# Performance work log

Measured on AMD Instinct MI355X. Metric: run time of the kernel, lower is better.

## Reference

```python
import jax, jax.numpy as jnp
import numpy as np

N, D, F, E, TOP_K = 8192, 1024, 2048, 8, 2


def setup_inputs() -> dict:
    key = jax.random.key(0)
    ks = jax.random.split(key, 8)
    s = 0.02
    x = jax.random.normal(ks[0], (N, D), dtype=jnp.float32)
    Wr = jax.random.normal(ks[1], (D, E), dtype=jnp.float32) * s  # router
    br = jnp.zeros((E,), jnp.float32)
    W1 = jax.random.normal(ks[2], (E, D, F), dtype=jnp.float32) * s  # expert FFN in
    b1 = jnp.zeros((E, F), jnp.float32)
    W2 = jax.random.normal(ks[3], (E, F, D), dtype=jnp.float32) * s  # expert FFN out
    b2 = jnp.zeros((E, D), jnp. float32)
    return {"x": x, "Wr": Wr, "br": br, "W1": W1, "b1": b1, "W2": W2, "b2": b2}


def reference(x, Wr, br, W1, b1, W2, b2):
    # Router: per-token expert logits -> softmax probabilities -> top-k sampler.
    logits = x @ Wr + br                         # [N, E]
    probs = jax.nn.softmax(logits, axis=-1)      # [N, E]
    top_p, top_i = jax.lax.top_k(probs, TOP_K)   # [N, K]
    # Combine weights: prob mass only on the selected top-k experts per token.
    w = (jax.nn.one_hot(top_i, E, dtype=x.dtype) * top_p[..., None]).sum(axis=1)  # [N, E]
    # Per-expert gather-compute-scatter, expressed as masked full-batch expert FFN
    # (identical math: tokens not routed to expert e have weight 0).
    out = jnp.zeros((x.shape[0], W2.shape[-1]), dtype=x.dtype)
    for e in range(E):  # small fixed loop over structurally distinct experts
        h = jax.nn.gelu(x @ W1[e] + b1[e])       # [N, F]
        y = h @ W2[e] + b2[e]                    # [N, D]
        out = out + w[:, e:e + 1] * y            # weighted scatter-add combine
    return out
```

## Files before the change

### kernel.cpp

```cpp
#include <hip/hip_runtime.h>
#include <hip/hip_bf16.h>


#define N_TOK 8192
#define DIM   1024
#define FF    2048
#define NE    8

typedef unsigned short ushort_t;
typedef __bf16 bf16x8 __attribute__((ext_vector_type(8)));
typedef float  f32x4  __attribute__((ext_vector_type(4)));
typedef unsigned short u16x8 __attribute__((ext_vector_type(8)));

__device__ __forceinline__ ushort_t f2bf(float f) {
    union { float f; unsigned int u; } v; v.f = f;
    unsigned int r = (v.u + 0x7FFFu + ((v.u >> 16) & 1u)) >> 16;
    return (ushort_t)r;
}

__device__ __forceinline__ void gload_lds16(const ushort_t* g, ushort_t* l) {
    __builtin_amdgcn_global_load_lds(
        (const __attribute__((address_space(1))) void*)g,
        (__attribute__((address_space(3))) void*)l,
        16, 0, 0);
}

__global__ __launch_bounds__(256) void convert_x_kernel(
    const float* __restrict__ x, ushort_t* __restrict__ xb)
{
    size_t i = ((size_t)blockIdx.x * 256 + threadIdx.x) * 8;
    float4 a = *reinterpret_cast<const float4*>(x + i);
    float4 b = *reinterpret_cast<const float4*>(x + i + 4);
    u16x8 o;
    o[0] = f2bf(a.x); o[1] = f2bf(a.y); o[2] = f2bf(a.z); o[3] = f2bf(a.w);
    o[4] = f2bf(b.x); o[5] = f2bf(b.y); o[6] = f2bf(b.z); o[7] = f2bf(b.w);
    *reinterpret_cast<u16x8*>(xb + i) = o;
}

__global__ __launch_bounds__(256) void transpose_conv_kernel(
    const float* __restrict__ in, ushort_t* __restrict__ out, int R, int C)
{
    __shared__ float tile[64][68];
    const int e = blockIdx.z;
    const float* I = in + (size_t)e * R * C;
    ushort_t*    O = out + (size_t)e * R * C;
    const int c0 = blockIdx.x * 64, r0 = blockIdx.y * 64;
    const int tid = threadIdx.x;
#pragma unroll
    for (int j = 0; j < 4; ++j) {
        int row = j * 16 + (tid >> 4);
        int col = (tid & 15) * 4;
        float4 v = *reinterpret_cast<const float4*>(&I[(size_t)(r0 + row) * C + c0 + col]);
        *reinterpret_cast<float4*>(&tile[row][col]) = v;
    }
    __syncthreads();
#pragma unroll
    for (int j = 0; j < 2; ++j) {
        int orow = j * 32 + (tid >> 3);
        int k0   = (tid & 7) * 8;
        u16x8 o;
#pragma unroll
        for (int k = 0; k < 8; ++k) o[k] = f2bf(tile[k0 + k][orow]);
        *reinterpret_cast<u16x8*>(&O[(size_t)(c0 + orow) * R + r0 + k0]) = o;
    }
}

__global__ __launch_bounds__(256) void router_kernel(
    const float* __restrict__ x, const float* __restrict__ Wr, const float* __restrict__ br,
    int* __restrict__ cnt, int* __restrict__ tok_list, float* __restrict__ w_list)
{
    __shared__ int   se0[64], se1[64];
    __shared__ float sw0[64], sw1[64];

    const int wid  = threadIdx.x >> 6;
    const int lane = threadIdx.x & 63;
    const int tblk = blockIdx.x * 64;

    for (int i = 0; i < 16; ++i) {
        const int li = wid * 16 + i;
        const int t  = tblk + li;
        const float* xr = x + (size_t)t * DIM;

        float acc[NE];
#pragma unroll
        for (int e = 0; e < NE; ++e) acc[e] = 0.f;
        for (int d = lane; d < DIM; d += 64) {
            float xv = xr[d];
            const float4* w4 = reinterpret_cast<const float4*>(Wr + (size_t)d * NE);
            float4 w0 = w4[0], w1 = w4[1];
            acc[0] += xv * w0.x; acc[1] += xv * w0.y; acc[2] += xv * w0.z; acc[3] += xv * w0.w;
            acc[4] += xv * w1.x; acc[5] += xv * w1.y; acc[6] += xv * w1.z; acc[7] += xv * w1.w;
        }
#pragma unroll
        for (int e = 0; e < NE; ++e) {
            for (int off = 32; off > 0; off >>= 1)
                acc[e] += __shfl_down(acc[e], off, 64);
        }
        if (lane == 0) {
            float l[NE];
#pragma unroll
            for (int e = 0; e < NE; ++e) l[e] = acc[e] + br[e];
            float mx = l[0];
#pragma unroll
            for (int e = 1; e < NE; ++e) mx = fmaxf(mx, l[e]);
            float p[NE], s = 0.f;
#pragma unroll
            for (int e = 0; e < NE; ++e) { p[e] = expf(l[e] - mx); s += p[e]; }
            float inv = 1.f / s;
            int e0 = 0;
#pragma unroll
            for (int e = 1; e < NE; ++e) if (l[e] > l[e0]) e0 = e;
            int e1 = (e0 == 0) ? 1 : 0;
#pragma unroll
            for (int e = 0; e < NE; ++e) if (e != e0 && l[e] > l[e1]) e1 = e;
            se0[li] = e0; sw0[li] = p[e0] * inv;
            se1[li] = e1; sw1[li] = p[e1] * inv;
        }
    }
    __syncthreads();

    if (threadIdx.x < 64) {
        const int t  = tblk + lane;
        const int e0 = se0[lane], e1 = se1[lane];
        const unsigned long long below = ((unsigned long long)1 << lane) - 1;
        int p0 = 0, p1 = 0;
#pragma unroll
        for (int e = 0; e < NE; ++e) {
            unsigned long long m0 = __ballot(e0 == e);
            unsigned long long m1 = __ballot(e1 == e);
            int c = __popcll(m0) + __popcll(m1);
            int b = 0;
            if (lane == e && c) b = atomicAdd(&cnt[e], c);
            b = __shfl(b, e, 64);
            if (e0 == e) p0 = b + __popcll(m0 & below);
            if (e1 == e) p1 = b + __popcll(m0) + __popcll(m1 & below);
        }
        tok_list[e0 * N_TOK + p0] = t;  w_list[e0 * N_TOK + p0] = sw0[lane];
        tok_list[e1 * N_TOK + p1] = t;  w_list[e1 * N_TOK + p1] = sw1[lane];
    }
}

__global__ void scan_kernel(const int* __restrict__ cnt, int* __restrict__ offs,
                            int* __restrict__ tile_e, int* __restrict__ tile_m0,
                            int* __restrict__ meta)
{
    if (threadIdx.x == 0 && blockIdx.x == 0) {
        int s = 0;
        for (int e = 0; e < NE; ++e) { offs[e] = s; s += cnt[e]; }
        offs[NE] = s;
        int nt = 0;
        for (int e = 0; e < NE; ++e)
            for (int m0 = 0; m0 < cnt[e]; m0 += 128) {
                tile_e[nt] = e; tile_m0[nt] = m0; ++nt;
            }
        meta[0] = nt;
    }
}

template <int MODE>
__global__ __launch_bounds__(512, 6) void moe_gemm_kernel(
    const ushort_t* __restrict__ A,
    const ushort_t* __restrict__ Bt,
    const float*    __restrict__ bias,
    const int*      __restrict__ cnt,
    const int*      __restrict__ offs,
    const int*      __restrict__ tok_list,
    const float*    __restrict__ w_list,
    const int*      __restrict__ tile_e,
    const int*      __restrict__ tile_m0,
    const int*      __restrict__ meta,
    ushort_t*       __restrict__ hout,
    float*          __restrict__ out)
{
    const int K    = (MODE == 0) ? 1024 : 2048;
    const int NCOL = (MODE == 0) ? 2048 : 1024;

    const int nmt = meta[0];
    const int L   = nmt << 4;

    const int xcd = blockIdx.x & 7;
    const int q = L >> 3, r = L & 7;
    const int cstart = (xcd < r) ? xcd * (q + 1) : r * (q + 1) + (xcd - r) * q;
    const int clen   = (xcd < r) ? q + 1 : q;

    __shared__ ushort_t As[3][128 * 32];
    __shared__ ushort_t Bs[3][128 * 32];

    const int tid  = threadIdx.x;
    const int lane = tid & 63;
    const int wid  = tid >> 6;
    const int wr = (wid >> 2) * 64;
    const int wc = (wid & 3) * 32;
    const int la = lane & 15;
    const int kc = lane >> 4;

    for (int i = blockIdx.x >> 3; i < clen; i += 96) {
        const int tau = cstart + i;
        const int mt  = tau >> 4;
        int nb, kh;
        if (MODE == 0) { nb = tau & 15; kh = 0; }
        else           { kh = tau & 1;  nb = (tau >> 1) & 7; }
        const int e   = tile_e[mt];
        const int m0  = tile_m0[mt];
        const int cnt_e  = cnt[e];
        const int offs_e = offs[e];
        const int n0  = nb * 128;
        const int koff = kh << 10;

        __syncthreads();

        const int srow  = tid >> 2;
        const int chunk = (tid & 3) ^ ((srow >> 1) & 3);
        size_t asrc, bsrc;
        {
            int entry = m0 + srow;
            if (MODE == 0) {
                int tok = (entry < cnt_e) ? tok_list[e * N_TOK + entry] : 0;
                asrc = (size_t)tok * K + chunk * 8;
            } else {
                asrc = (size_t)(offs_e + entry) * K + koff + chunk * 8;
            }
            bsrc = ((size_t)e * NCOL + n0 + srow) * K + koff + chunk * 8;
        }

        f32x4 acc[4][2];
#pragma unroll
        for (int m = 0; m < 4; ++m)
#pragma unroll
            for (int n = 0; n < 2; ++n)
                acc[m][n] = (f32x4){0.f, 0.f, 0.f, 0.f};

        auto STAGE = [&](int t, int b) {
            int k0 = t * 32;
            gload_lds16(A  + asrc + k0, &As[b][tid * 8]);
            gload_lds16(Bt + bsrc + k0, &Bs[b][tid * 8]);
        };

        auto COMPUTE = [&](int b) {
            bf16x8 af[4], bfr[2];
#pragma unroll
            for (int m = 0; m < 4; ++m) {
                int rr = wr + m * 16 + la;
                af[m] = *reinterpret_cast<const bf16x8*>(&As[b][(rr * 4 + (kc ^ ((rr >> 1) & 3))) * 8]);
            }
#pragma unroll
            for (int n = 0; n < 2; ++n) {
                int rr = wc + n * 16 + la;
                bfr[n] = *reinterpret_cast<const bf16x8*>(&Bs[b][(rr * 4 + (kc ^ ((rr >> 1) & 3))) * 8]);
            }
            __builtin_amdgcn_s_setprio(1);
#pragma unroll
            for (int m = 0; m < 4; ++m)
#pragma unroll
                for (int n = 0; n < 2; ++n)
                    acc[m][n] = __builtin_amdgcn_mfma_f32_16x16x32_bf16(af[m], bfr[n], acc[m][n], 0, 0, 0);
            __builtin_amdgcn_s_setprio(0);
        };

        const int nk = 32;
        STAGE(0, 0);
        STAGE(1, 1);
        for (int t = 0; t < nk - 1; ++t) {
            asm volatile("s_waitcnt vmcnt(2)" ::: "memory");
            __builtin_amdgcn_s_barrier();
            if (t + 2 < nk) STAGE(t + 2, (t + 2) % 3);
            COMPUTE(t % 3);
        }
        asm volatile("s_waitcnt vmcnt(0)" ::: "memory");
        __builtin_amdgcn_s_barrier();
        COMPUTE((nk - 1) % 3);

#pragma unroll
        for (int m = 0; m < 4; ++m) {
            int rbase = wr + m * 16 + (lane >> 4) * 4;
#pragma unroll
            for (int n = 0; n < 2; ++n) {
                int gcol = n0 + wc + n * 16 + la;
                float bi = (MODE == 1 && kh != 0) ? 0.f : bias[(size_t)e * NCOL + gcol];
#pragma unroll
                for (int jj = 0; jj < 4; ++jj) {
                    int entry = m0 + rbase + jj;
                    if (entry < cnt_e) {
                        float v = acc[m][n][jj] + bi;
                        if (MODE == 0) {
                            float u = 0.7978845608028654f * (v + 0.044715f * v * v * v);
                            float t2 = __builtin_amdgcn_exp2f(2.8853900817779268f * u);
                            float g = v * (t2 / (t2 + 1.f));
                            hout[(size_t)(offs_e + entry) * FF + gcol] = f2bf(g);
                        } else {
                            int tok  = tok_list[e * N_TOK + entry];
                            float w  = w_list  [e * N_TOK + entry];
                            atomicAdd(&out[(size_t)tok * DIM + gcol], w * v);
                        }
                    }
                }
            }
        }
    }
}

extern "C" void kernel_launch(void* const* d_in, const int* in_sizes, int n_in,
                              void* d_out, int out_size, void* d_ws, size_t ws_size,
                              hipStream_t stream)
{
    const float* x  = (const float*)d_in[0];
    const float* Wr = (const float*)d_in[1];
    const float* br = (const float*)d_in[2];
    const float* W1 = (const float*)d_in[3];
    const float* b1 = (const float*)d_in[4];
    const float* W2 = (const float*)d_in[5];
    const float* b2 = (const float*)d_in[6];
    float* out = (float*)d_out;

    char* ws = (char*)d_ws;
    size_t off = 0;
    auto alloc = [&](size_t bytes) -> void* {
        void* p = ws + off;
        off = (off + bytes + 255) & ~(size_t)255;
        return p;
    };
    ushort_t* w1t = (ushort_t*)alloc((size_t)NE * DIM * FF * 2);
    ushort_t* w2t = (ushort_t*)alloc((size_t)NE * DIM * FF * 2);
    ushort_t* xb  = (ushort_t*)alloc((size_t)N_TOK * DIM * 2);
    ushort_t* h   = (ushort_t*)alloc(((size_t)2 * N_TOK + 128) * FF * 2);
    int*      cnt = (int*)alloc(NE * sizeof(int));
    int*      offs= (int*)alloc((NE + 1) * sizeof(int));
    int*   tok_list = (int*)alloc((size_t)NE * N_TOK * sizeof(int));
    float* w_list   = (float*)alloc((size_t)NE * N_TOK * sizeof(float));
    int*   tile_e   = (int*)alloc(256 * sizeof(int));
    int*   tile_m0  = (int*)alloc(256 * sizeof(int));
    int*   meta     = (int*)alloc(16 * sizeof(int));
    (void)ws_size; (void)in_sizes; (void)n_in;

    hipMemsetAsync(out, 0, (size_t)out_size * sizeof(float), stream);
    hipMemsetAsync(cnt, 0, NE * sizeof(int), stream);

    convert_x_kernel<<<(N_TOK * DIM) / (8 * 256), 256, 0, stream>>>(x, xb);
    transpose_conv_kernel<<<dim3(FF / 64, DIM / 64, NE), 256, 0, stream>>>(W1, w1t, DIM, FF);
    transpose_conv_kernel<<<dim3(DIM / 64, FF / 64, NE), 256, 0, stream>>>(W2, w2t, FF, DIM);
    router_kernel<<<N_TOK / 64, 256, 0, stream>>>(x, Wr, br, cnt, tok_list, w_list);
    scan_kernel<<<1, 64, 0, stream>>>(cnt, offs, tile_e, tile_m0, meta);

    moe_gemm_kernel<0><<<768, 512, 0, stream>>>(
        xb, w1t, b1, cnt, offs, tok_list, w_list, tile_e, tile_m0, meta, h, nullptr);
    moe_gemm_kernel<1><<<768, 512, 0, stream>>>(
        h, w2t, b2, cnt, offs, tok_list, w_list, tile_e, tile_m0, meta, nullptr, out);
}
```

Measured before the change: 453.9 us.

## Enlarge MoE GEMM tiles to 256x256x64 with double-buffered phased MFMA schedule

Increases the expert GEMM block tile from 128x128 (K-step 32) to 256x256 (K-step 64), so each wave computes a 128x64 sub-tile with 32 accumulators. The old 3-stage ring is replaced by two LDS buffers and a four-phase schedule that interleaves the next tile's global-to-LDS loads with MFMA phases, separated by explicit barriers. Grid size drops to 256 persistent blocks (one per CU), and the router tile list and h padding grow to match 256-row tiles. The aim is more operand reuse per LDS byte and less global traffic per FLOP. The cost is higher register and LDS pressure at one block per CU, plus more wasted work on partially filled 256-row expert tiles.

Result: slower. 661.2 us (+45.7%).

```diff
diff --git a/kernel.cpp b/kernel.cpp
--- a/kernel.cpp
+++ b/kernel.cpp
@@ -150,7 +150,7 @@
         offs[NE] = s;
         int nt = 0;
         for (int e = 0; e < NE; ++e)
-            for (int m0 = 0; m0 < cnt[e]; m0 += 128) {
+            for (int m0 = 0; m0 < cnt[e]; m0 += 256) {
                 tile_e[nt] = e; tile_m0[nt] = m0; ++nt;
             }
         meta[0] = nt;
@@ -158,7 +158,7 @@
 }
 
 template <int MODE>
-__global__ __launch_bounds__(512, 6) void moe_gemm_kernel(
+__global__ __launch_bounds__(512, 1) void moe_gemm_kernel(
     const ushort_t* __restrict__ A,
     const ushort_t* __restrict__ Bt,
     const float*    __restrict__ bias,
@@ -176,105 +176,144 @@
     const int NCOL = (MODE == 0) ? 2048 : 1024;
 
     const int nmt = meta[0];
-    const int L   = nmt << 4;
+    const int L   = nmt << 3;
 
     const int xcd = blockIdx.x & 7;
     const int q = L >> 3, r = L & 7;
     const int cstart = (xcd < r) ? xcd * (q + 1) : r * (q + 1) + (xcd - r) * q;
     const int clen   = (xcd < r) ? q + 1 : q;
 
-    __shared__ ushort_t As[3][128 * 32];
-    __shared__ ushort_t Bs[3][128 * 32];
+    __shared__ ushort_t As0[256 * 64];
+    __shared__ ushort_t Bs0[256 * 64];
+    __shared__ ushort_t As1[256 * 64];
+    __shared__ ushort_t Bs1[256 * 64];
 
     const int tid  = threadIdx.x;
     const int lane = tid & 63;
     const int wid  = tid >> 6;
-    const int wr = (wid >> 2) * 64;
-    const int wc = (wid & 3) * 32;
+    const int wr = (wid >> 2) * 128;
+    const int wc = (wid & 3) * 64;
     const int la = lane & 15;
     const int kc = lane >> 4;
 
-    for (int i = blockIdx.x >> 3; i < clen; i += 96) {
+    for (int i = blockIdx.x >> 3; i < clen; i += 32) {
         const int tau = cstart + i;
-        const int mt  = tau >> 4;
+        const int mt  = tau >> 3;
         int nb, kh;
-        if (MODE == 0) { nb = tau & 15; kh = 0; }
-        else           { kh = tau & 1;  nb = (tau >> 1) & 7; }
+        if (MODE == 0) { nb = tau & 7; kh = 0; }
+        else           { kh = tau & 1; nb = (tau >> 1) & 3; }
         const int e   = tile_e[mt];
         const int m0  = tile_m0[mt];
         const int cnt_e  = cnt[e];
         const int offs_e = offs[e];
-        const int n0  = nb * 128;
+        const int n0  = nb * 256;
         const int koff = kh << 10;
 
-        __syncthreads();
-
-        const int srow  = tid >> 2;
-        const int chunk = (tid & 3) ^ ((srow >> 1) & 3);
-        size_t asrc, bsrc;
-        {
-            int entry = m0 + srow;
+        size_t asrc[4], bsrc[4];
+#pragma unroll
+        for (int j = 0; j < 4; ++j) {
+            int c = tid + 512 * j;
+            int row = c >> 3;
+            int gch = (c & 7) ^ (row & 7);
+            int entry = m0 + row;
+            size_t arow;
             if (MODE == 0) {
                 int tok = (entry < cnt_e) ? tok_list[e * N_TOK + entry] : 0;
-                asrc = (size_t)tok * K + chunk * 8;
+                arow = (size_t)tok * K;
             } else {
-                asrc = (size_t)(offs_e + entry) * K + koff + chunk * 8;
+                arow = (size_t)(offs_e + entry) * K;
             }
-            bsrc = ((size_t)e * NCOL + n0 + srow) * K + koff + chunk * 8;
-        }
-
-        f32x4 acc[4][2];
-#pragma unroll
-        for (int m = 0; m < 4; ++m)
-#pragma unroll
-            for (int n = 0; n < 2; ++n)
+            asrc[j] = arow + koff + (size_t)gch * 8;
+            int col = n0 + row;
+            bsrc[j] = ((size_t)e * NCOL + col) * K + koff + (size_t)gch * 8;
+        }
+
+        f32x4 acc[8][4];
+#pragma unroll
+        for (int m = 0; m < 8; ++m)
+#pragma unroll
+            for (int n = 0; n < 4; ++n)
                 acc[m][n] = (f32x4){0.f, 0.f, 0.f, 0.f};
 
-        auto STAGE = [&](int t, int b) {
-            int k0 = t * 32;
-            gload_lds16(A  + asrc + k0, &As[b][tid * 8]);
-            gload_lds16(Bt + bsrc + k0, &Bs[b][tid * 8]);
+        auto STAGE_A = [&](int t, ushort_t* dst) {
+            const int k0 = t * 64;
+#pragma unroll
+            for (int j = 0; j < 4; ++j)
+                gload_lds16(A + asrc[j] + k0, &dst[(tid + 512 * j) * 8]);
         };
-
-        auto COMPUTE = [&](int b) {
-            bf16x8 af[4], bfr[2];
-#pragma unroll
-            for (int m = 0; m < 4; ++m) {
-                int rr = wr + m * 16 + la;
-                af[m] = *reinterpret_cast<const bf16x8*>(&As[b][(rr * 4 + (kc ^ ((rr >> 1) & 3))) * 8]);
-            }
-#pragma unroll
-            for (int n = 0; n < 2; ++n) {
-                int rr = wc + n * 16 + la;
-                bfr[n] = *reinterpret_cast<const bf16x8*>(&Bs[b][(rr * 4 + (kc ^ ((rr >> 1) & 3))) * 8]);
-            }
-            __builtin_amdgcn_s_setprio(1);
-#pragma unroll
-            for (int m = 0; m < 4; ++m)
-#pragma unroll
-                for (int n = 0; n < 2; ++n)
-                    acc[m][n] = __builtin_amdgcn_mfma_f32_16x16x32_bf16(af[m], bfr[n], acc[m][n], 0, 0, 0);
-            __builtin_amdgcn_s_setprio(0);
+        auto STAGE_B = [&](int t, ushort_t* dst) {
+            const int k0 = t * 64;
+#pragma unroll
+            for (int j = 0; j < 4; ++j)
+                gload_lds16(Bt + bsrc[j] + k0, &dst[(tid + 512 * j) * 8]);
         };
 
-        const int nk = 32;
-        STAGE(0, 0);
-        STAGE(1, 1);
-        for (int t = 0; t < nk - 1; ++t) {
-            asm volatile("s_waitcnt vmcnt(2)" ::: "memory");
-            __builtin_amdgcn_s_barrier();
-            if (t + 2 < nk) STAGE(t + 2, (t + 2) % 3);
-            COMPUTE(t % 3);
-        }
-        asm volatile("s_waitcnt vmcnt(0)" ::: "memory");
-        __builtin_amdgcn_s_barrier();
-        COMPUTE((nk - 1) % 3);
-
-#pragma unroll
-        for (int m = 0; m < 4; ++m) {
+        const int nt = 16;
+
+#define PHASE(MH, S, STG, CA, CB, NA, NB)                                      \
+        {                                                                      \
+            bf16x8 af[4], bf[4];                                               \
+            _Pragma("unroll")                                                  \
+            for (int m = 0; m < 4; ++m) {                                      \
+                int rr = wr + ((MH) * 4 + m) * 16 + la;                        \
+                af[m] = *reinterpret_cast<const bf16x8*>(                      \
+                    &CA[(rr * 8 + (((S) * 4 + kc) ^ (rr & 7))) * 8]);          \
+            }                                                                  \
+            _Pragma("unroll")                                                  \
+            for (int n = 0; n < 4; ++n) {                                      \
+                int cc = wc + n * 16 + la;                                     \
+                bf[n] = *reinterpret_cast<const bf16x8*>(                      \
+                    &CB[(cc * 8 + (((S) * 4 + kc) ^ (cc & 7))) * 8]);          \
+            }                                                                  \
+            if ((STG) == 1 && has_next) STAGE_A(tn, NA);                       \
+            if ((STG) == 2 && has_next) STAGE_B(tn, NB);                       \
+            __builtin_amdgcn_s_barrier();                                      \
+            asm volatile("s_waitcnt lgkmcnt(0)" ::: "memory");                 \
+            __builtin_amdgcn_sched_barrier(0);                                 \
+            __builtin_amdgcn_s_setprio(1);                                     \
+            _Pragma("unroll")                                                  \
+            for (int m = 0; m < 4; ++m)                                        \
+                _Pragma("unroll")                                              \
+                for (int n = 0; n < 4; ++n)                                    \
+                    acc[(MH) * 4 + m][n] = __builtin_amdgcn_mfma_f32_16x16x32_bf16( \
+                        af[m], bf[n], acc[(MH) * 4 + m][n], 0, 0, 0);          \
+            __builtin_amdgcn_s_setprio(0);                                     \
+            __builtin_amdgcn_s_barrier();                                      \
+        }
+
+#define TILE(T, CA, CB, NA, NB)                                                \
+        {                                                                      \
+            const int tn = (T) + 1;                                            \
+            const bool has_next = tn < nt;                                     \
+            PHASE(0, 0, 1, CA, CB, NA, NB)                                     \
+            PHASE(1, 0, 2, CA, CB, NA, NB)                                     \
+            PHASE(0, 1, 0, CA, CB, NA, NB)                                     \
+            PHASE(1, 1, 0, CA, CB, NA, NB)                                     \
+        }
+
+#define VMB() do {                                                             \
+            asm volatile("s_waitcnt vmcnt(0)" ::: "memory");                   \
+            __builtin_amdgcn_s_barrier();                                      \
+        } while (0)
+
+        STAGE_A(0, As0);
+        STAGE_B(0, Bs0);
+        VMB();
+        for (int tt = 0; tt < nt; tt += 2) {
+            TILE(tt,     As0, Bs0, As1, Bs1);
+            VMB();
+            TILE(tt + 1, As1, Bs1, As0, Bs0);
+            VMB();
+        }
+#undef PHASE
+#undef TILE
+#undef VMB
+
+#pragma unroll
+        for (int m = 0; m < 8; ++m) {
             int rbase = wr + m * 16 + (lane >> 4) * 4;
 #pragma unroll
-            for (int n = 0; n < 2; ++n) {
+            for (int n = 0; n < 4; ++n) {
                 int gcol = n0 + wc + n * 16 + la;
                 float bi = (MODE == 1 && kh != 0) ? 0.f : bias[(size_t)e * NCOL + gcol];
 #pragma unroll
@@ -322,7 +361,7 @@
     ushort_t* w1t = (ushort_t*)alloc((size_t)NE * DIM * FF * 2);
     ushort_t* w2t = (ushort_t*)alloc((size_t)NE * DIM * FF * 2);
     ushort_t* xb  = (ushort_t*)alloc((size_t)N_TOK * DIM * 2);
-    ushort_t* h   = (ushort_t*)alloc(((size_t)2 * N_TOK + 128) * FF * 2);
+    ushort_t* h   = (ushort_t*)alloc(((size_t)2 * N_TOK + 256) * FF * 2);
     int*      cnt = (int*)alloc(NE * sizeof(int));
     int*      offs= (int*)alloc((NE + 1) * sizeof(int));
     int*   tok_list = (int*)alloc((size_t)NE * N_TOK * sizeof(int));
@@ -341,8 +380,8 @@
     router_kernel<<<N_TOK / 64, 256, 0, stream>>>(x, Wr, br, cnt, tok_list, w_list);
     scan_kernel<<<1, 64, 0, stream>>>(cnt, offs, tile_e, tile_m0, meta);
 
-    moe_gemm_kernel<0><<<768, 512, 0, stream>>>(
+    moe_gemm_kernel<0><<<256, 512, 0, stream>>>(
         xb, w1t, b1, cnt, offs, tok_list, w_list, tile_e, tile_m0, meta, h, nullptr);
-    moe_gemm_kernel<1><<<768, 512, 0, stream>>>(
+    moe_gemm_kernel<1><<<256, 512, 0, stream>>>(
         h, w2t, b2, cnt, offs, tok_list, w_list, tile_e, tile_m0, meta, nullptr, out);
 }
```

## Use 4-wave blocks with 64x64 warp tiles and double-buffered LDS in MoE GEMM

Applied to the files above, without the earlier changes.

Each MoE GEMM block shrinks from 8 waves to 4, and every wave now computes a 64x64 sub-tile (4x4 MFMAs) rather than 64x32. This raises register-level reuse of the A and B fragments per LDS read. The 3-stage LDS pipeline with an explicit vmcnt wait is replaced by a ping-pong double buffer using full __syncthreads, and the grid becomes 1024 blocks. The fp32-to-bf16 conversion kernels now use packed bf16x2 intrinsics. The trade-off is more accumulator registers per thread, lower occupancy and a shallower prefetch depth, which may expose more memory latency.

Measured after the change: 495.8 us. 1.09x slower.

```diff
diff --git a/kernel.cpp b/kernel.cpp
--- a/kernel.cpp
+++ b/kernel.cpp
@@ -16,6 +16,11 @@
     union { float f; unsigned int u; } v; v.f = f;
     unsigned int r = (v.u + 0x7FFFu + ((v.u >> 16) & 1u)) >> 16;
     return (ushort_t)r;
+}
+
+__device__ __forceinline__ unsigned int pkbf2(float lo, float hi) {
+    __hip_bfloat162 h = __float22bfloat162_rn(make_float2(lo, hi));
+    return *reinterpret_cast<unsigned int*>(&h);
 }
 
 __device__ __forceinline__ void gload_lds16(const ushort_t* g, ushort_t* l) {
@@ -31,10 +36,10 @@
     size_t i = ((size_t)blockIdx.x * 256 + threadIdx.x) * 8;
     float4 a = *reinterpret_cast<const float4*>(x + i);
     float4 b = *reinterpret_cast<const float4*>(x + i + 4);
-    u16x8 o;
-    o[0] = f2bf(a.x); o[1] = f2bf(a.y); o[2] = f2bf(a.z); o[3] = f2bf(a.w);
-    o[4] = f2bf(b.x); o[5] = f2bf(b.y); o[6] = f2bf(b.z); o[7] = f2bf(b.w);
-    *reinterpret_cast<u16x8*>(xb + i) = o;
+    uint4 o;
+    o.x = pkbf2(a.x, a.y); o.y = pkbf2(a.z, a.w);
+    o.z = pkbf2(b.x, b.y); o.w = pkbf2(b.z, b.w);
+    *reinterpret_cast<uint4*>(xb + i) = o;
 }
 
 __global__ __launch_bounds__(256) void transpose_conv_kernel(
@@ -58,10 +63,12 @@
     for (int j = 0; j < 2; ++j) {
         int orow = j * 32 + (tid >> 3);
         int k0   = (tid & 7) * 8;
-        u16x8 o;
-#pragma unroll
-        for (int k = 0; k < 8; ++k) o[k] = f2bf(tile[k0 + k][orow]);
-        *reinterpret_cast<u16x8*>(&O[(size_t)(c0 + orow) * R + r0 + k0]) = o;
+        uint4 o;
+        o.x = pkbf2(tile[k0 + 0][orow], tile[k0 + 1][orow]);
+        o.y = pkbf2(tile[k0 + 2][orow], tile[k0 + 3][orow]);
+        o.z = pkbf2(tile[k0 + 4][orow], tile[k0 + 5][orow]);
+        o.w = pkbf2(tile[k0 + 6][orow], tile[k0 + 7][orow]);
+        *reinterpret_cast<uint4*>(&O[(size_t)(c0 + orow) * R + r0 + k0]) = o;
     }
 }
 
@@ -158,7 +165,7 @@
 }
 
 template <int MODE>
-__global__ __launch_bounds__(512, 6) void moe_gemm_kernel(
+__global__ __launch_bounds__(256, 4) void moe_gemm_kernel(
     const ushort_t* __restrict__ A,
     const ushort_t* __restrict__ Bt,
     const float*    __restrict__ bias,
@@ -183,18 +190,20 @@
     const int cstart = (xcd < r) ? xcd * (q + 1) : r * (q + 1) + (xcd - r) * q;
     const int clen   = (xcd < r) ? q + 1 : q;
 
-    __shared__ ushort_t As[3][128 * 32];
-    __shared__ ushort_t Bs[3][128 * 32];
+    __shared__ ushort_t As0[128 * 32];
+    __shared__ ushort_t Bs0[128 * 32];
+    __shared__ ushort_t As1[128 * 32];
+    __shared__ ushort_t Bs1[128 * 32];
 
     const int tid  = threadIdx.x;
     const int lane = tid & 63;
     const int wid  = tid >> 6;
-    const int wr = (wid >> 2) * 64;
-    const int wc = (wid & 3) * 32;
+    const int wr = (wid >> 1) * 64;
+    const int wc = (wid & 1) * 64;
     const int la = lane & 15;
     const int kc = lane >> 4;
 
-    for (int i = blockIdx.x >> 3; i < clen; i += 96) {
+    for (int i = blockIdx.x >> 3; i < clen; i += 128) {
         const int tau = cstart + i;
         const int mt  = tau >> 4;
         int nb, kh;
@@ -209,72 +218,79 @@
 
         __syncthreads();
 
-        const int srow  = tid >> 2;
-        const int chunk = (tid & 3) ^ ((srow >> 1) & 3);
-        size_t asrc, bsrc;
-        {
-            int entry = m0 + srow;
+        size_t asrc[2], bsrc[2];
+#pragma unroll
+        for (int j = 0; j < 2; ++j) {
+            int c = tid + 256 * j;
+            int row   = c >> 2;
+            int chunk = (c & 3) ^ ((row >> 1) & 3);
+            int entry = m0 + row;
+            size_t arow;
             if (MODE == 0) {
                 int tok = (entry < cnt_e) ? tok_list[e * N_TOK + entry] : 0;
-                asrc = (size_t)tok * K + chunk * 8;
+                arow = (size_t)tok * K;
             } else {
-                asrc = (size_t)(offs_e + entry) * K + koff + chunk * 8;
-            }
-            bsrc = ((size_t)e * NCOL + n0 + srow) * K + koff + chunk * 8;
-        }
-
-        f32x4 acc[4][2];
+                arow = (size_t)(offs_e + entry) * K;
+            }
+            asrc[j] = arow + koff + (size_t)chunk * 8;
+            int col = n0 + row;
+            bsrc[j] = ((size_t)e * NCOL + col) * K + koff + (size_t)chunk * 8;
+        }
+
+        f32x4 acc[4][4];
 #pragma unroll
         for (int m = 0; m < 4; ++m)
 #pragma unroll
-            for (int n = 0; n < 2; ++n)
+            for (int n = 0; n < 4; ++n)
                 acc[m][n] = (f32x4){0.f, 0.f, 0.f, 0.f};
 
-        auto STAGE = [&](int t, int b) {
+        auto STAGE = [&](int t, ushort_t* Ad, ushort_t* Bd) {
             int k0 = t * 32;
-            gload_lds16(A  + asrc + k0, &As[b][tid * 8]);
-            gload_lds16(Bt + bsrc + k0, &Bs[b][tid * 8]);
+#pragma unroll
+            for (int j = 0; j < 2; ++j) {
+                gload_lds16(A  + asrc[j] + k0, &Ad[(tid + 256 * j) * 8]);
+                gload_lds16(Bt + bsrc[j] + k0, &Bd[(tid + 256 * j) * 8]);
+            }
         };
 
-        auto COMPUTE = [&](int b) {
-            bf16x8 af[4], bfr[2];
+        auto COMPUTE = [&](const ushort_t* Ad, const ushort_t* Bd) {
+            bf16x8 af[4], bfr[4];
 #pragma unroll
             for (int m = 0; m < 4; ++m) {
                 int rr = wr + m * 16 + la;
-                af[m] = *reinterpret_cast<const bf16x8*>(&As[b][(rr * 4 + (kc ^ ((rr >> 1) & 3))) * 8]);
-            }
-#pragma unroll
-            for (int n = 0; n < 2; ++n) {
+                af[m] = *reinterpret_cast<const bf16x8*>(&Ad[(rr * 4 + (kc ^ ((rr >> 1) & 3))) * 8]);
+            }
+#pragma unroll
+            for (int n = 0; n < 4; ++n) {
                 int rr = wc + n * 16 + la;
-                bfr[n] = *reinterpret_cast<const bf16x8*>(&Bs[b][(rr * 4 + (kc ^ ((rr >> 1) & 3))) * 8]);
+                bfr[n] = *reinterpret_cast<const bf16x8*>(&Bd[(rr * 4 + (kc ^ ((rr >> 1) & 3))) * 8]);
             }
             __builtin_amdgcn_s_setprio(1);
 #pragma unroll
             for (int m = 0; m < 4; ++m)
 #pragma unroll
-                for (int n = 0; n < 2; ++n)
+                for (int n = 0; n < 4; ++n)
                     acc[m][n] = __builtin_amdgcn_mfma_f32_16x16x32_bf16(af[m], bfr[n], acc[m][n], 0, 0, 0);
             __builtin_amdgcn_s_setprio(0);
         };
 
         const int nk = 32;
-        STAGE(0, 0);
-        STAGE(1, 1);
-        for (int t = 0; t < nk - 1; ++t) {
-            asm volatile("s_waitcnt vmcnt(2)" ::: "memory");
-            __builtin_amdgcn_s_barrier();
-            if (t + 2 < nk) STAGE(t + 2, (t + 2) % 3);
-            COMPUTE(t % 3);
-        }
-        asm volatile("s_waitcnt vmcnt(0)" ::: "memory");
-        __builtin_amdgcn_s_barrier();
-        COMPUTE((nk - 1) % 3);
+        STAGE(0, As0, Bs0);
+        __syncthreads();
+        for (int t = 0; t < nk; t += 2) {
+            if (t + 1 < nk) STAGE(t + 1, As1, Bs1);
+            COMPUTE(As0, Bs0);
+            __syncthreads();
+            if (t + 2 < nk) STAGE(t + 2, As0, Bs0);
+            COMPUTE(As1, Bs1);
+            __syncthreads();
+        }
 
 #pragma unroll
         for (int m = 0; m < 4; ++m) {
             int rbase = wr + m * 16 + (lane >> 4) * 4;
 #pragma unroll
-            for (int n = 0; n < 2; ++n) {
+            for (int n = 0; n < 4; ++n) {
                 int gcol = n0 + wc + n * 16 + la;
                 float bi = (MODE == 1 && kh != 0) ? 0.f : bias[(size_t)e * NCOL + gcol];
 #pragma unroll
@@ -341,8 +357,8 @@
     router_kernel<<<N_TOK / 64, 256, 0, stream>>>(x, Wr, br, cnt, tok_list, w_list);
     scan_kernel<<<1, 64, 0, stream>>>(cnt, offs, tile_e, tile_m0, meta);
 
-    moe_gemm_kernel<0><<<768, 512, 0, stream>>>(
+    moe_gemm_kernel<0><<<1024, 256, 0, stream>>>(
         xb, w1t, b1, cnt, offs, tok_list, w_list, tile_e, tile_m0, meta, h, nullptr);
-    moe_gemm_kernel<1><<<768, 512, 0, stream>>>(
+    moe_gemm_kernel<1><<<1024, 256, 0, stream>>>(
         h, w2t, b2, cnt, offs, tok_list, w_list, tile_e, tile_m0, meta, nullptr, out);
 }
```
